# Optimization experiments

Hardware: AMD Instinct MI355X
Metric: run time of the kernel (lower is better)

## Reference

```python
import jax, jax.numpy as jnp
import numpy as np

B = 2097152   # batch
Z = 16        # z_dim
K = 64        # num_hidden_nodes


def setup_inputs() -> dict:
    key = jax.random.key(0)
    k1, k2, k3, k4, k5 = jax.random.split(key, 5)
    return {
        "z": jax.random.normal(k1, (B, Z), dtype=jnp.float32),
        "a_0": jax.random.normal(k2, (1,), dtype=jnp.float32),
        "bk": jax.random.normal(k3, (K,), dtype=jnp.float32),
        "ck": jax.random.normal(k4, (K, Z), dtype=jnp.float32),
        "dk": jax.random.normal(k5, (K,), dtype=jnp.float32),
    }


def reference(z, a_0, bk, ck, dk):
    # Vectorized over the batch: y[b] = a_0 + sum_k bk[k] * tanh((ck @ z[b])[k] + dk[k])
    h = jnp.tanh(jnp.einsum("bz,kz->bk", z, ck) + dk)  # [B, K]
    y = a_0 + h @ bk                                     # [B]
    return y[:, None]                                     # [B, 1]
```

## Files before the change

kernel.cpp:

```cpp
#include <hip/hip_runtime.h>
#include <stdint.h>

typedef __attribute__((ext_vector_type(8)))  short  short8;
typedef __attribute__((ext_vector_type(8)))  __bf16 bf16x8;
typedef __attribute__((ext_vector_type(16))) float  floatx16;
typedef __attribute__((ext_vector_type(4)))  float  floatx4;
typedef __attribute__((ext_vector_type(2)))  float  float2v;
typedef __attribute__((ext_vector_type(4)))  uint32_t uint4v;

union Frag { short8 s; bf16x8 v; uint4v d; };
union FU   { float f; uint32_t u; };

__device__ __forceinline__ short f2bf(float f) {
    FU x; x.f = f;
    uint32_t r = x.u + 0x7fffu + ((x.u >> 16) & 1u);
    return (short)(r >> 16);
}

__device__ __forceinline__ uint32_t pack_bf2(float lo, float hi) {
    FU a, b; a.f = lo; b.f = hi;
    return __builtin_amdgcn_perm(b.u + 0x8000u, a.u + 0x8000u, 0x07060302u);
}

__device__ __forceinline__ float fexp2(float x) { return __builtin_amdgcn_exp2f(x); }
__device__ __forceinline__ float frcp(float x)  { return __builtin_amdgcn_rcpf(x); }
__device__ __forceinline__ float fclamp(float x, float lo, float hi) {
#if __has_builtin(__builtin_amdgcn_fmed3f)
    return __builtin_amdgcn_fmed3f(x, lo, hi);
#else
    return fminf(fmaxf(x, lo), hi);
#endif
}

__device__ __forceinline__ float2v tpair(float a, float b) {
    float2v t;
    t.x = fexp2(fclamp(a, -30.0f, 30.0f));
    t.y = fexp2(fclamp(b, -30.0f, 30.0f));
    return t + 1.0f;
}

__global__ __launch_bounds__(256) void mave_kernel(
    const float* __restrict__ z,
    const float* __restrict__ a0,
    const float* __restrict__ bk,
    const float* __restrict__ ck,
    const float* __restrict__ dk,
    float* __restrict__ out,
    int ntiles)
{
    const int lane = threadIdx.x & 63;
    const int m    = lane & 31;
    const int g    = lane >> 5;
    const float S  = 2.885390081777927f;

    const int wid   = (int)((blockIdx.x * blockDim.x + threadIdx.x) >> 6);
    const int tile0 = wid * 4;
    if (tile0 >= ntiles) return;
    const int tlast = ntiles - 1;

    floatx4 zb[4][2];
    {
        const float* zp = z + (size_t)m * 16 + g * 8;
        #pragma unroll
        for (int i = 0; i < 4; ++i) {
            int ti = tile0 + i; if (ti > tlast) ti = tlast;
            const float* q = zp + (size_t)ti * 512;
            zb[i][0] = *(const floatx4*)q;
            zb[i][1] = *(const floatx4*)(q + 4);
        }
    }

    Frag af0, af1;
    {
        const float* c0 = ck + m * 16 + g * 8;
        const float* c1 = c0 + 32 * 16;
        #pragma unroll
        for (int e = 0; e < 8; ++e) {
            af0.s[e] = f2bf(c0[e] * S);
            af1.s[e] = f2bf(c1[e] * S);
        }
    }
    floatx16 cinit0, cinit1;
    uint32_t nbp[16];
    #pragma unroll
    for (int r = 0; r < 16; ++r) {
        int n = (r & 3) + 8 * (r >> 2) + 4 * g;
        cinit0[r] = S * dk[n];
        cinit1[r] = S * dk[n + 32];
        nbp[r] = pack_bf2(-2.0f * bk[n], -2.0f * bk[n + 32]);
    }
    float base = a0[0];
    for (int k = 0; k < 64; ++k) base += bk[k];

    #pragma unroll
    for (int i = 0; i < 4; ++i) {
        Frag bfr;
        bfr.d[0] = pack_bf2(zb[i][0].x, zb[i][0].y);
        bfr.d[1] = pack_bf2(zb[i][0].z, zb[i][0].w);
        bfr.d[2] = pack_bf2(zb[i][1].x, zb[i][1].y);
        bfr.d[3] = pack_bf2(zb[i][1].z, zb[i][1].w);

        floatx16 acc0 = __builtin_amdgcn_mfma_f32_32x32x16_bf16(af0.v, bfr.v, cinit0, 0, 0, 0);
        floatx16 acc1 = __builtin_amdgcn_mfma_f32_32x32x16_bf16(af1.v, bfr.v, cinit1, 0, 0, 0);

        float2v Ya = {0.0f, 0.0f}, Yb = {0.0f, 0.0f};
        #pragma unroll
        for (int r = 0; r < 16; r += 4) {
            float2v T0 = tpair(acc0[r+0], acc1[r+0]);
            float2v T1 = tpair(acc0[r+1], acc1[r+1]);
            float2v T2 = tpair(acc0[r+2], acc1[r+2]);
            float2v T3 = tpair(acc0[r+3], acc1[r+3]);
            float2v P01 = T0 * T1, P23 = T2 * T3, P = P01 * P23;
            float2v R; R.x = frcp(P.x); R.y = frcp(P.y);
            FU l0, h0, l1, h1, l2, h2, l3, h3;
            l0.u = nbp[r+0] << 16; h0.u = nbp[r+0] & 0xffff0000u;
            l1.u = nbp[r+1] << 16; h1.u = nbp[r+1] & 0xffff0000u;
            l2.u = nbp[r+2] << 16; h2.u = nbp[r+2] & 0xffff0000u;
            l3.u = nbp[r+3] << 16; h3.u = nbp[r+3] & 0xffff0000u;
            float2v nb0 = {l0.f, h0.f}, nb1 = {l1.f, h1.f};
            float2v nb2 = {l2.f, h2.f}, nb3 = {l3.f, h3.f};
            float2v n01 = nb0 * T1 + nb1 * T0;
            float2v n23 = nb2 * T3 + nb3 * T2;
            float2v num = n01 * P23 + n23 * P01;
            if (r & 4) Yb += num * R; else Ya += num * R;
        }
        float2v Yv = Ya + Yb;
        float y = Yv.x + Yv.y;
        y += __shfl_xor(y, 32, 64);
        int ti = tile0 + i; if (ti > tlast) ti = tlast;
        if (g == 0) out[ti * 32 + m] = base + y;
    }
}

extern "C" void kernel_launch(void* const* d_in, const int* in_sizes, int n_in,
                              void* d_out, int out_size, void* d_ws, size_t ws_size,
                              hipStream_t stream) {
    const float* z  = (const float*)d_in[0];
    const float* a0 = (const float*)d_in[1];
    const float* bk = (const float*)d_in[2];
    const float* ck = (const float*)d_in[3];
    const float* dk = (const float*)d_in[4];
    float* out = (float*)d_out;

    const int B      = in_sizes[0] / 16;
    const int ntiles = B / 32;

    const int blocks = (ntiles + 15) / 16;
    hipLaunchKernelGGL(mave_kernel, dim3(blocks), dim3(256), 0, stream,
                       z, a0, bk, ck, dk, out, ntiles);
}
```

Before: 199.7 us.

## Process eight tiles per wave with rolling z prefetch and batched output stores

Each wave now handles eight 32-row tiles instead of four. A four-slot register ring prefetches the z data for tile i+4 while tile i is computed. Amortizing the per-wave setup (ck fragments, dk and bk constants, the base sum) over more tiles cuts redundant setup work. The bk weights are kept as full fp32 pairs instead of packed bf16, which removes the unpack shifts and masks but uses more registers. The shuffles and output stores are grouped after the loop. The risks are higher register pressure and only half as many waves to hide memory latency.

Result: no change. 198.1 us (-0.8%).

```diff
diff --git a/kernel.cpp b/kernel.cpp
--- a/kernel.cpp
+++ b/kernel.cpp
@@ -54,20 +54,19 @@
     const float S  = 2.885390081777927f;
 
     const int wid   = (int)((blockIdx.x * blockDim.x + threadIdx.x) >> 6);
-    const int tile0 = wid * 4;
+    const int tile0 = wid * 8;
     if (tile0 >= ntiles) return;
     const int tlast = ntiles - 1;
 
+    const float* zp = z + (size_t)m * 16 + g * 8;
+
     floatx4 zb[4][2];
-    {
-        const float* zp = z + (size_t)m * 16 + g * 8;
-        #pragma unroll
-        for (int i = 0; i < 4; ++i) {
-            int ti = tile0 + i; if (ti > tlast) ti = tlast;
-            const float* q = zp + (size_t)ti * 512;
-            zb[i][0] = *(const floatx4*)q;
-            zb[i][1] = *(const floatx4*)(q + 4);
-        }
+    #pragma unroll
+    for (int i = 0; i < 4; ++i) {
+        int ti = tile0 + i; if (ti > tlast) ti = tlast;
+        const float* q = zp + (size_t)ti * 512;
+        zb[i][0] = *(const floatx4*)q;
+        zb[i][1] = *(const floatx4*)(q + 4);
     }
 
     Frag af0, af1;
@@ -81,24 +80,35 @@
         }
     }
     floatx16 cinit0, cinit1;
-    uint32_t nbp[16];
+    float2v  nb2[16];
     #pragma unroll
     for (int r = 0; r < 16; ++r) {
         int n = (r & 3) + 8 * (r >> 2) + 4 * g;
         cinit0[r] = S * dk[n];
         cinit1[r] = S * dk[n + 32];
-        nbp[r] = pack_bf2(-2.0f * bk[n], -2.0f * bk[n + 32]);
+        nb2[r].x = -2.0f * bk[n];
+        nb2[r].y = -2.0f * bk[n + 32];
     }
     float base = a0[0];
     for (int k = 0; k < 64; ++k) base += bk[k];
 
+    float yv[8];
     #pragma unroll
-    for (int i = 0; i < 4; ++i) {
+    for (int i = 0; i < 8; ++i) {
+        const int s4 = i & 3;
+
         Frag bfr;
-        bfr.d[0] = pack_bf2(zb[i][0].x, zb[i][0].y);
-        bfr.d[1] = pack_bf2(zb[i][0].z, zb[i][0].w);
-        bfr.d[2] = pack_bf2(zb[i][1].x, zb[i][1].y);
-        bfr.d[3] = pack_bf2(zb[i][1].z, zb[i][1].w);
+        bfr.d[0] = pack_bf2(zb[s4][0].x, zb[s4][0].y);
+        bfr.d[1] = pack_bf2(zb[s4][0].z, zb[s4][0].w);
+        bfr.d[2] = pack_bf2(zb[s4][1].x, zb[s4][1].y);
+        bfr.d[3] = pack_bf2(zb[s4][1].z, zb[s4][1].w);
+
+        if (i + 4 < 8) {
+            int ti = tile0 + i + 4; if (ti > tlast) ti = tlast;
+            const float* q = zp + (size_t)ti * 512;
+            zb[s4][0] = *(const floatx4*)q;
+            zb[s4][1] = *(const floatx4*)(q + 4);
+        }
 
         floatx16 acc0 = __builtin_amdgcn_mfma_f32_32x32x16_bf16(af0.v, bfr.v, cinit0, 0, 0, 0);
         floatx16 acc1 = __builtin_amdgcn_mfma_f32_32x32x16_bf16(af1.v, bfr.v, cinit1, 0, 0, 0);
@@ -112,23 +122,24 @@
             float2v T3 = tpair(acc0[r+3], acc1[r+3]);
             float2v P01 = T0 * T1, P23 = T2 * T3, P = P01 * P23;
             float2v R; R.x = frcp(P.x); R.y = frcp(P.y);
-            FU l0, h0, l1, h1, l2, h2, l3, h3;
-            l0.u = nbp[r+0] << 16; h0.u = nbp[r+0] & 0xffff0000u;
-            l1.u = nbp[r+1] << 16; h1.u = nbp[r+1] & 0xffff0000u;
-            l2.u = nbp[r+2] << 16; h2.u = nbp[r+2] & 0xffff0000u;
-            l3.u = nbp[r+3] << 16; h3.u = nbp[r+3] & 0xffff0000u;
-            float2v nb0 = {l0.f, h0.f}, nb1 = {l1.f, h1.f};
-            float2v nb2 = {l2.f, h2.f}, nb3 = {l3.f, h3.f};
-            float2v n01 = nb0 * T1 + nb1 * T0;
-            float2v n23 = nb2 * T3 + nb3 * T2;
+            float2v n01 = nb2[r+0] * T1 + nb2[r+1] * T0;
+            float2v n23 = nb2[r+2] * T3 + nb2[r+3] * T2;
             float2v num = n01 * P23 + n23 * P01;
             if (r & 4) Yb += num * R; else Ya += num * R;
         }
         float2v Yv = Ya + Yb;
-        float y = Yv.x + Yv.y;
-        y += __shfl_xor(y, 32, 64);
-        int ti = tile0 + i; if (ti > tlast) ti = tlast;
-        if (g == 0) out[ti * 32 + m] = base + y;
+        yv[i] = Yv.x + Yv.y;
+    }
+
+    float ov[8];
+    #pragma unroll
+    for (int i = 0; i < 8; ++i) ov[i] = __shfl_xor(yv[i], 32, 64);
+    if (g == 0) {
+        #pragma unroll
+        for (int i = 0; i < 8; ++i) {
+            int ti = tile0 + i; if (ti > tlast) ti = tlast;
+            out[(size_t)ti * 32 + m] = base + yv[i] + ov[i];
+        }
     }
 }
 
@@ -145,7 +156,7 @@
     const int B      = in_sizes[0] / 16;
     const int ntiles = B / 32;
 
-    const int blocks = (ntiles + 15) / 16;
+    const int blocks = (ntiles + 31) / 32;
     hipLaunchKernelGGL(mave_kernel, dim3(blocks), dim3(256), 0, stream,
                        z, a0, bk, ck, dk, out, ntiles);
 }
```
